# Kernel tuning notes

Measured on AMD Instinct MI355X. Metric: run time of the kernel, lower is better.

## Reference

```python
import jax, jax.numpy as jnp
import numpy as np

HEAD = 8
DIM_IN = 512
PAD = (4, 4)            # pad = head - dim % head = 8 -> (4, 4)
DIM = DIM_IN + sum(PAD) # 520
DH = DIM // HEAD        # 65


def setup_inputs() -> dict:
    key = jax.random.key(0)
    k1, k2, k3, k4 = jax.random.split(key, 4)
    B, L = 4, 2048
    inp = jax.random.normal(k1, (B, L, DIM_IN), dtype=jnp.float32)
    # nn.Linear weights, shape (out, in), bias=False
    scale = 1.0 / np.sqrt(DIM)
    w_q = jax.random.uniform(k2, (DIM, DIM), jnp.float32, -scale, scale)
    w_k = jax.random.uniform(k3, (DIM, DIM), jnp.float32, -scale, scale)
    w_v = jax.random.uniform(k4, (DIM, DIM), jnp.float32, -scale, scale)
    return {"inp": inp, "w_q": w_q, "w_k": w_k, "w_v": w_v}


def reference(inp, w_q, w_k, w_v):
    # F.pad(inp, pad) pads the last (feature) dim
    x = jnp.pad(inp, ((0, 0), (0, 0), (PAD[0], PAD[1])))
    B, L, D = x.shape
    # project then split heads: [B, H, L, dh]
    def proj(w):
        return (x @ w.T).reshape(B, L, HEAD, DH).transpose(0, 2, 1, 3)
    q, k, v = proj(w_q), proj(w_k), proj(w_v)
    score = jnp.einsum('bhqd,bhkd->bhqk', q, k) / jnp.sqrt(jnp.float32(DH))
    attn = jax.nn.softmax(score, axis=-1)          # [B, H, L, L]
    # dropout is identity in eval/reference mode
    out = jnp.einsum('bhqk,bhkd->bhqd', attn, v)
    out = out.transpose(0, 2, 1, 3).reshape(B, L, D)
    out = out[:, :, PAD[0]:-PAD[1]]                # strip feature padding
    return out, attn
```

## Files before the change

kernel.cpp:

```cpp
#include <hip/hip_runtime.h>

typedef unsigned short u16;
typedef __bf16 bf16x8 __attribute__((ext_vector_type(8)));
typedef float f32x16 __attribute__((ext_vector_type(16)));
typedef unsigned short ushort8 __attribute__((ext_vector_type(8)));

#define LOG2E 1.44269504088896340736f
#define QSCALE 0.12403473458920846f

__device__ __forceinline__ u16 f2bf(float f) {
  unsigned u = __float_as_uint(f);
  u = (u + 0x7fffu + ((u >> 16) & 1u)) >> 16;
  return (u16)u;
}

__device__ __forceinline__ f32x16 zero16() {
  f32x16 z;
#pragma unroll
  for (int i = 0; i < 16; ++i) z[i] = 0.0f;
  return z;
}

__device__ __forceinline__ void gload_lds16(const u16* g, u16* l) {
  __builtin_amdgcn_global_load_lds(
      (const __attribute__((address_space(1))) void*)g,
      (__attribute__((address_space(3))) void*)l, 16, 0, 0);
}

__global__ __launch_bounds__(256) void cvt_x_kernel(const float4* __restrict__ in,
                                                    ushort4* __restrict__ out) {
  int i = blockIdx.x * 256 + threadIdx.x;
  float4 v = in[i];
  ushort4 o;
  o.x = f2bf(v.x); o.y = f2bf(v.y); o.z = f2bf(v.z); o.w = f2bf(v.w);
  out[i] = o;
}

__global__ __launch_bounds__(256) void cvt_w_kernel(const float* __restrict__ wq,
                                                    const float* __restrict__ wk,
                                                    const float* __restrict__ wv,
                                                    u16* __restrict__ wtt) {
  int id = blockIdx.x * 256 + threadIdx.x;
  int wsel = id / (544 * 512);
  int rem = id - wsel * (544 * 512);
  int j = rem >> 9, k = rem & 511;
  const float* wp = (wsel == 0) ? wq : (wsel == 1) ? wk : wv;
  float v = (j < 520) ? wp[j * 520 + k + 4] : 0.0f;
  wtt[id] = f2bf(v);
}

__global__ __launch_bounds__(256) void zero_kernel(uint4* __restrict__ p, int n) {
  int i = blockIdx.x * 256 + threadIdx.x;
  uint4 z = make_uint4(0u, 0u, 0u, 0u);
  for (; i < n; i += gridDim.x * 256) p[i] = z;
}

__global__ __launch_bounds__(256) void proj_kernel(const u16* __restrict__ xb,
                                                   const u16* __restrict__ wtt,
                                                   u16* __restrict__ qb,
                                                   u16* __restrict__ kpl,
                                                   u16* __restrict__ vb) {
  int tid = threadIdx.x;
  int w = tid >> 6, l = tid & 63, lr = l & 31, lh = l >> 5;
  int m0 = blockIdx.y * 128 + w * 32;
  int g = blockIdx.x;

  const u16* ap = xb + (size_t)(m0 + lr) * 512 + lh * 8;

  f32x16 acc[4];
  const u16* bp[4];
  bool valid[4];
#pragma unroll
  for (int i = 0; i < 4; ++i) {
    int nt = g * 4 + i;
    valid[i] = (nt < 51);
    int ntc = valid[i] ? nt : 50;
    bp[i] = wtt + ((size_t)((ntc / 17) * 544 + (ntc % 17) * 32) + lr) * 512 + lh * 8;
    acc[i] = zero16();
  }

#pragma unroll 4
  for (int s = 0; s < 32; ++s) {
    bf16x8 a = *reinterpret_cast<const bf16x8*>(ap + s * 16);
#pragma unroll
    for (int i = 0; i < 4; ++i) {
      if (valid[i]) {
        bf16x8 b = *reinterpret_cast<const bf16x8*>(bp[i] + s * 16);
        acc[i] = __builtin_amdgcn_mfma_f32_32x32x16_bf16(a, b, acc[i], 0, 0, 0);
      }
    }
  }

#pragma unroll
  for (int i = 0; i < 4; ++i) {
    int nt = g * 4 + i;
    if (nt < 51) {
      int wsel = nt / 17;
      int j = (nt % 17) * 32 + lr;
      if (j < 520) {
        int h = j / 65, dh = j - h * 65;
#pragma unroll
        for (int r = 0; r < 16; ++r) {
          int m = m0 + (r & 3) + 8 * (r >> 2) + 4 * lh;
          int bb = m >> 11, lrow = m & 2047;
          int bh = bb * 8 + h;
          if (wsel == 0) {
            qb[((size_t)bh * 2048 + lrow) * 80 + dh] = f2bf(acc[i][r] * QSCALE);
          } else if (wsel == 1) {
            kpl[(((size_t)bh * 10 + (dh >> 3)) * 2048 + lrow) * 8 + (dh & 7)] = f2bf(acc[i][r]);
          } else {
            vb[((size_t)bh * 2048 + lrow) * 80 + dh] = f2bf(acc[i][r]);
          }
        }
      }
    }
  }
}

__global__ __launch_bounds__(256) void repack_v_kernel(const u16* __restrict__ vb,
                                                       u16* __restrict__ vpl) {
  __shared__ u16 lds[256 * 88];
  int bh = blockIdx.y;
  int key0 = blockIdx.x * 256;
  int t = threadIdx.x;

  const u16* src = vb + ((size_t)bh * 2048 + key0) * 80;
#pragma unroll
  for (int i = 0; i < 10; ++i) {
    int f16 = i * 256 + t;
    int row = f16 / 10, col = f16 % 10;
    ushort8 v = *reinterpret_cast<const ushort8*>(src + f16 * 8);
    *reinterpret_cast<ushort8*>(&lds[row * 88 + col * 8]) = v;
  }
  __syncthreads();

#pragma unroll
  for (int j = 0; j < 10; ++j) {
    int slot = j * 256 + t;
    int kc = slot / 80, d = slot - kc * 80;
    ushort8 v;
#pragma unroll
    for (int e = 0; e < 8; ++e) v[e] = lds[(kc * 8 + e) * 88 + d];
    *reinterpret_cast<ushort8*>(
        &vpl[(((size_t)bh * 256 + (key0 >> 3) + kc) * 80 + d) * 8]) = v;
  }
}

__global__ __launch_bounds__(512) void attn_kernel(const u16* __restrict__ qb,
                                                   const u16* __restrict__ kpl,
                                                   const u16* __restrict__ vpl,
                                                   float* __restrict__ out,
                                                   float* __restrict__ attn) {
  __shared__ u16 kvbuf[2][10240];
  __shared__ u16 plds[8][32][40];

  int b = blockIdx.x;
  int bh = (b & 7) + 8 * (b >> 6);
  int qblk = (b >> 3) & 7;
  int tid = threadIdx.x;
  int w = tid >> 6, l = tid & 63, lr = l & 31, lh = l >> 5;
  int q0 = qblk * 256 + w * 32;

  const u16* kbh = kpl + (size_t)bh * 163840;
  const u16* vbh = vpl + (size_t)bh * 163840;

  const u16* qptr = qb + ((size_t)bh * 2048 + q0 + lr) * 80 + lh * 8;
  bf16x8 qf[5];
#pragma unroll
  for (int s = 0; s < 5; ++s) qf[s] = *reinterpret_cast<const bf16x8*>(qptr + s * 16);

  float sum[16];
#pragma unroll
  for (int r2 = 0; r2 < 16; ++r2) sum[r2] = 0.0f;

#define STAGE_K128(kt, bufi)                                                  \
  {                                                                           \
    _Pragma("unroll")                                                         \
    for (int i = 0; i < 3; ++i) {                                             \
      int idx = w + i * 8;                                                    \
      if (idx < 20) {                                                         \
        int c = idx >> 1, half = idx & 1;                                     \
        gload_lds16(kbh + (size_t)c * 16384 + (kt) * 1024 + half * 512 + l * 8, \
                    &kvbuf[bufi][idx * 512]);                                 \
      }                                                                       \
    }                                                                         \
  }

  STAGE_K128(0, 0);
  __syncthreads();
  int buf = 0;
  for (int t = 0; t < 16; ++t) {
    if (t < 15) STAGE_K128(t + 1, buf ^ 1);
#pragma unroll
    for (int sub = 0; sub < 4; ++sub) {
      f32x16 acc = zero16();
#pragma unroll
      for (int s = 0; s < 5; ++s) {
        bf16x8 bk = *reinterpret_cast<const bf16x8*>(
            &kvbuf[buf][((2 * s + lh) * 128 + sub * 32 + lr) * 8]);
        acc = __builtin_amdgcn_mfma_f32_32x32x16_bf16(qf[s], bk, acc, 0, 0, 0);
      }
#pragma unroll
      for (int r2 = 0; r2 < 16; ++r2)
        sum[r2] += __builtin_amdgcn_exp2f(acc[r2] * LOG2E);
    }
    __syncthreads();
    buf ^= 1;
  }

#pragma unroll
  for (int r2 = 0; r2 < 16; ++r2) {
    float s = sum[r2];
#pragma unroll
    for (int d = 1; d < 32; d <<= 1) s += __shfl_xor(s, d);
    sum[r2] = 1.0f / s;
  }

#define STAGE_KV64(t64, bufi)                                                 \
  {                                                                           \
    _Pragma("unroll")                                                         \
    for (int i = 0; i < 3; ++i) {                                             \
      int idx = w + i * 8;                                                    \
      if (idx < 20) {                                                         \
        const u16* src = (idx < 10)                                           \
            ? kbh + (size_t)idx * 16384 + (t64) * 512 + l * 8                 \
            : vbh + (size_t)(t64) * 5120 + (idx - 10) * 512 + l * 8;          \
        gload_lds16(src, &kvbuf[bufi][idx * 512]);                            \
      }                                                                       \
    }                                                                         \
  }

  f32x16 O[3];
#pragma unroll
  for (int n = 0; n < 3; ++n) O[n] = zero16();

  float* attn_base = attn + ((size_t)bh * 2048 + q0) * 2048;

  STAGE_KV64(0, 0);
  __syncthreads();
  buf = 0;
  for (int t = 0; t < 32; ++t) {
    if (t < 31) STAGE_KV64(t + 1, buf ^ 1);
#pragma unroll
    for (int sub = 0; sub < 2; ++sub) {
      int key0 = t * 64 + sub * 32;
      f32x16 acc = zero16();
#pragma unroll
      for (int s = 0; s < 5; ++s) {
        bf16x8 bk = *reinterpret_cast<const bf16x8*>(
            &kvbuf[buf][((2 * s + lh) * 64 + sub * 32 + lr) * 8]);
        acc = __builtin_amdgcn_mfma_f32_32x32x16_bf16(qf[s], bk, acc, 0, 0, 0);
      }
#pragma unroll
      for (int r2 = 0; r2 < 16; ++r2) {
        int row = (r2 & 3) + 8 * (r2 >> 2) + 4 * lh;
        float p = __builtin_amdgcn_exp2f(acc[r2] * LOG2E) * sum[r2];
        __builtin_nontemporal_store(p, &attn_base[(size_t)row * 2048 + key0 + lr]);
        plds[w][row][lr] = f2bf(p);
      }
#pragma unroll
      for (int ks = 0; ks < 2; ++ks) {
        bf16x8 pa = *reinterpret_cast<const bf16x8*>(&plds[w][lr][ks * 16 + lh * 8]);
#pragma unroll
        for (int n = 0; n < 3; ++n) {
          bf16x8 bv = *reinterpret_cast<const bf16x8*>(
              &kvbuf[buf][5120 + ((sub * 4 + 2 * ks + lh) * 80 + n * 32 + lr) * 8]);
          O[n] = __builtin_amdgcn_mfma_f32_32x32x16_bf16(pa, bv, O[n], 0, 0, 0);
        }
      }
    }
    __syncthreads();
    buf ^= 1;
  }

  int bb = bh >> 3, h = bh & 7;
#pragma unroll
  for (int n = 0; n < 3; ++n) {
    int d = n * 32 + lr;
    int cc = h * 65 + d - 4;
    if (d < 65 && cc >= 0 && cc < 512) {
#pragma unroll
      for (int r2 = 0; r2 < 16; ++r2) {
        int row = (r2 & 3) + 8 * (r2 >> 2) + 4 * lh;
        out[((size_t)bb * 2048 + q0 + row) * 512 + cc] = O[n][r2];
      }
    }
  }
}

extern "C" void kernel_launch(void* const* d_in, const int* in_sizes, int n_in,
                              void* d_out, int out_size, void* d_ws, size_t ws_size,
                              hipStream_t stream) {
  (void)in_sizes; (void)n_in; (void)out_size; (void)ws_size;
  const float* inp = (const float*)d_in[0];
  const float* wq  = (const float*)d_in[1];
  const float* wk  = (const float*)d_in[2];
  const float* wv  = (const float*)d_in[3];

  char* ws = (char*)d_ws;
  u16* xb  = (u16*)(ws + 0);
  u16* wtt = (u16*)(ws + 8388608);
  u16* qb  = (u16*)(ws + 10059776);
  u16* kpl = (u16*)(ws + 20545536);
  u16* vb  = (u16*)(ws + 31031296);
  u16* vpl = (u16*)(ws + 41517056);

  float* out  = (float*)d_out;
  float* attn = out + (size_t)4 * 2048 * 512;

  cvt_x_kernel<<<4096, 256, 0, stream>>>((const float4*)inp, (ushort4*)xb);
  cvt_w_kernel<<<3264, 256, 0, stream>>>(wq, wk, wv, wtt);
  zero_kernel<<<640, 256, 0, stream>>>((uint4*)qb, 655360);
  proj_kernel<<<dim3(13, 64), 256, 0, stream>>>(xb, wtt, qb, kpl, vb);
  repack_v_kernel<<<dim3(8, 32), 256, 0, stream>>>(vb, vpl);
  attn_kernel<<<256, 512, 0, stream>>>(qb, kpl, vpl, out, attn);
}
```

Before: 286.2 us.

## Fuse V repack into projection, fold log2e into Q scale, relax attention barriers

```diff
diff --git a/kernel.cpp b/kernel.cpp
--- a/kernel.cpp
+++ b/kernel.cpp
@@ -5,8 +5,7 @@
 typedef float f32x16 __attribute__((ext_vector_type(16)));
 typedef unsigned short ushort8 __attribute__((ext_vector_type(8)));
 
-#define LOG2E 1.44269504088896340736f
-#define QSCALE 0.12403473458920846f
+#define QSCALE2 0.17894429680154087f
 
 __device__ __forceinline__ u16 f2bf(float f) {
   unsigned u = __float_as_uint(f);
@@ -59,7 +58,7 @@
                                                    const u16* __restrict__ wtt,
                                                    u16* __restrict__ qb,
                                                    u16* __restrict__ kpl,
-                                                   u16* __restrict__ vb) {
+                                                   u16* __restrict__ vpl) {
   int tid = threadIdx.x;
   int w = tid >> 6, l = tid & 63, lr = l & 31, lh = l >> 5;
   int m0 = blockIdx.y * 128 + w * 32;
@@ -99,17 +98,32 @@
       int j = (nt % 17) * 32 + lr;
       if (j < 520) {
         int h = j / 65, dh = j - h * 65;
-#pragma unroll
-        for (int r = 0; r < 16; ++r) {
-          int m = m0 + (r & 3) + 8 * (r >> 2) + 4 * lh;
-          int bb = m >> 11, lrow = m & 2047;
-          int bh = bb * 8 + h;
-          if (wsel == 0) {
-            qb[((size_t)bh * 2048 + lrow) * 80 + dh] = f2bf(acc[i][r] * QSCALE);
-          } else if (wsel == 1) {
-            kpl[(((size_t)bh * 10 + (dh >> 3)) * 2048 + lrow) * 8 + (dh & 7)] = f2bf(acc[i][r]);
-          } else {
-            vb[((size_t)bh * 2048 + lrow) * 80 + dh] = f2bf(acc[i][r]);
+        if (wsel == 2) {
+#pragma unroll
+          for (int g2 = 0; g2 < 4; ++g2) {
+            int m = m0 + g2 * 8 + 4 * lh;
+            int bb = m >> 11, lrow = m & 2047;
+            int bh = bb * 8 + h;
+            int kc = lrow >> 3;
+            ushort4 vv;
+            vv.x = f2bf(acc[i][4 * g2]);
+            vv.y = f2bf(acc[i][4 * g2 + 1]);
+            vv.z = f2bf(acc[i][4 * g2 + 2]);
+            vv.w = f2bf(acc[i][4 * g2 + 3]);
+            *reinterpret_cast<ushort4*>(
+                &vpl[(((size_t)bh * 256 + kc) * 80 + dh) * 8 + 4 * lh]) = vv;
+          }
+        } else {
+#pragma unroll
+          for (int r = 0; r < 16; ++r) {
+            int m = m0 + (r & 3) + 8 * (r >> 2) + 4 * lh;
+            int bb = m >> 11, lrow = m & 2047;
+            int bh = bb * 8 + h;
+            if (wsel == 0) {
+              qb[((size_t)bh * 2048 + lrow) * 80 + dh] = f2bf(acc[i][r] * QSCALE2);
+            } else {
+              kpl[(((size_t)bh * 10 + (dh >> 3)) * 2048 + lrow) * 8 + (dh & 7)] = f2bf(acc[i][r]);
+            }
           }
         }
       }
@@ -117,40 +131,11 @@
   }
 }
 
-__global__ __launch_bounds__(256) void repack_v_kernel(const u16* __restrict__ vb,
-                                                       u16* __restrict__ vpl) {
-  __shared__ u16 lds[256 * 88];
-  int bh = blockIdx.y;
-  int key0 = blockIdx.x * 256;
-  int t = threadIdx.x;
-
-  const u16* src = vb + ((size_t)bh * 2048 + key0) * 80;
-#pragma unroll
-  for (int i = 0; i < 10; ++i) {
-    int f16 = i * 256 + t;
-    int row = f16 / 10, col = f16 % 10;
-    ushort8 v = *reinterpret_cast<const ushort8*>(src + f16 * 8);
-    *reinterpret_cast<ushort8*>(&lds[row * 88 + col * 8]) = v;
-  }
-  __syncthreads();
-
-#pragma unroll
-  for (int j = 0; j < 10; ++j) {
-    int slot = j * 256 + t;
-    int kc = slot / 80, d = slot - kc * 80;
-    ushort8 v;
-#pragma unroll
-    for (int e = 0; e < 8; ++e) v[e] = lds[(kc * 8 + e) * 88 + d];
-    *reinterpret_cast<ushort8*>(
-        &vpl[(((size_t)bh * 256 + (key0 >> 3) + kc) * 80 + d) * 8]) = v;
-  }
-}
-
-__global__ __launch_bounds__(512) void attn_kernel(const u16* __restrict__ qb,
-                                                   const u16* __restrict__ kpl,
-                                                   const u16* __restrict__ vpl,
-                                                   float* __restrict__ out,
-                                                   float* __restrict__ attn) {
+__global__ __launch_bounds__(512, 4) void attn_kernel(const u16* __restrict__ qb,
+                                                      const u16* __restrict__ kpl,
+                                                      const u16* __restrict__ vpl,
+                                                      float* __restrict__ out,
+                                                      float* __restrict__ attn) {
   __shared__ u16 kvbuf[2][10240];
   __shared__ u16 plds[8][32][40];
 
@@ -160,6 +145,7 @@
   int tid = threadIdx.x;
   int w = tid >> 6, l = tid & 63, lr = l & 31, lh = l >> 5;
   int q0 = qblk * 256 + w * 32;
+  int phase = (b * 11) & 31;
 
   const u16* kbh = kpl + (size_t)bh * 163840;
   const u16* vbh = vpl + (size_t)bh * 163840;
@@ -202,7 +188,7 @@
       }
 #pragma unroll
       for (int r2 = 0; r2 < 16; ++r2)
-        sum[r2] += __builtin_amdgcn_exp2f(acc[r2] * LOG2E);
+        sum[r2] += __builtin_amdgcn_exp2f(acc[r2]);
     }
     __syncthreads();
     buf ^= 1;
@@ -236,14 +222,15 @@
 
   float* attn_base = attn + ((size_t)bh * 2048 + q0) * 2048;
 
-  STAGE_KV64(0, 0);
+  STAGE_KV64(phase, 0);
   __syncthreads();
   buf = 0;
   for (int t = 0; t < 32; ++t) {
-    if (t < 31) STAGE_KV64(t + 1, buf ^ 1);
+    int tt = (t + phase) & 31;
+    if (t < 31) STAGE_KV64((tt + 1) & 31, buf ^ 1);
 #pragma unroll
     for (int sub = 0; sub < 2; ++sub) {
-      int key0 = t * 64 + sub * 32;
+      int key0 = tt * 64 + sub * 32;
       f32x16 acc = zero16();
 #pragma unroll
       for (int s = 0; s < 5; ++s) {
@@ -254,7 +241,7 @@
 #pragma unroll
       for (int r2 = 0; r2 < 16; ++r2) {
         int row = (r2 & 3) + 8 * (r2 >> 2) + 4 * lh;
-        float p = __builtin_amdgcn_exp2f(acc[r2] * LOG2E) * sum[r2];
+        float p = __builtin_amdgcn_exp2f(acc[r2]) * sum[r2];
         __builtin_nontemporal_store(p, &attn_base[(size_t)row * 2048 + key0 + lr]);
         plds[w][row][lr] = f2bf(p);
       }
@@ -269,7 +256,8 @@
         }
       }
     }
-    __syncthreads();
+    asm volatile("s_waitcnt vmcnt(32)" ::: "memory");
+    __builtin_amdgcn_s_barrier();
     buf ^= 1;
   }
 
@@ -302,8 +290,7 @@
   u16* wtt = (u16*)(ws + 8388608);
   u16* qb  = (u16*)(ws + 10059776);
   u16* kpl = (u16*)(ws + 20545536);
-  u16* vb  = (u16*)(ws + 31031296);
-  u16* vpl = (u16*)(ws + 41517056);
+  u16* vpl = (u16*)(ws + 31031296);
 
   float* out  = (float*)d_out;
   float* attn = out + (size_t)4 * 2048 * 512;
@@ -311,7 +298,6 @@
   cvt_x_kernel<<<4096, 256, 0, stream>>>((const float4*)inp, (ushort4*)xb);
   cvt_w_kernel<<<3264, 256, 0, stream>>>(wq, wk, wv, wtt);
   zero_kernel<<<640, 256, 0, stream>>>((uint4*)qb, 655360);
-  proj_kernel<<<dim3(13, 64), 256, 0, stream>>>(xb, wtt, qb, kpl, vb);
-  repack_v_kernel<<<dim3(8, 32), 256, 0, stream>>>(vb, vpl);
+  proj_kernel<<<dim3(13, 64), 256, 0, stream>>>(xb, wtt, qb, kpl, vpl);
   attn_kernel<<<256, 512, 0, stream>>>(qb, kpl, vpl, out, attn);
 }
```

New measurement: 622.0 us. +117.3%, slower.
